# Performance work log

Hardware: AMD Instinct MI355X
Metric: run time of the kernel (lower is better)

Reference implementation:

```python
import jax, jax.numpy as jnp
import numpy as np

EPS_LN = 1e-5

def layer_norm(x, w, b):
    u = x.mean(-1, keepdims=True)
    s = jnp.mean((x - u) ** 2, -1, keepdims=True)
    return w * ((x - u) / jnp.sqrt(s + EPS_LN)) + b

def mlp(x, W, b, lw, lb):
    return jax.nn.relu(layer_norm(x @ W + b, lw, lb))

def mlp_gate(x, W, b, lw, lb):
    return jax.nn.sigmoid(layer_norm(x @ W + b, lw, lb))

def setup_inputs() -> dict:
    N, D = 768, 64
    key = jax.random.key(0)
    ks = jax.random.split(key, 12)
    inp = {
        'corr_index': jax.random.normal(ks[0], (N, N, 2), jnp.float32),
        'nei_index': jax.random.randint(ks[1], (N, N), 0, 2).astype(jnp.int64),
        'nei_num': jax.random.randint(ks[2], (N,), 0, N).astype(jnp.int64),
        'hidden_state': jax.random.normal(ks[3], (N, D), jnp.float32),
        'agent_v': jax.random.normal(ks[4], (N, 2), jnp.float32),
        # relativeLayer: MLP(3, D)
        'rel_w': jax.random.normal(ks[5], (3, D), jnp.float32) * (1.0 / np.sqrt(3)),
        'rel_b': jnp.zeros((D,), jnp.float32),
        'rel_lw': jnp.ones((D,), jnp.float32),
        'rel_lb': jnp.zeros((D,), jnp.float32),
        # ngate: MLP_gate(3D, D)
        'ng_w': jax.random.normal(ks[6], (3 * D, D), jnp.float32) * (1.0 / np.sqrt(3 * D)),
        'ng_b': jnp.zeros((D,), jnp.float32),
        'ng_lw': jnp.ones((D,), jnp.float32),
        'ng_lb': jnp.zeros((D,), jnp.float32),
        # WAr: MLP(3D, 1) -- LayerNorm(1) is identity in the source
        'war_w': jax.random.normal(ks[7], (3 * D, 1), jnp.float32) * (1.0 / np.sqrt(3 * D)),
        'war_b': jnp.zeros((1,), jnp.float32),
        # weight: MLP(D, D)
        'wt_w': jax.random.normal(ks[8], (D, D), jnp.float32) * (1.0 / np.sqrt(D)),
        'wt_b': jnp.zeros((D,), jnp.float32),
        'wt_lw': jnp.ones((D,), jnp.float32),
        'wt_lb': jnp.zeros((D,), jnp.float32),
    }
    return inp

def reference(corr_index, nei_index, nei_num, hidden_state, agent_v,
              rel_w, rel_b, rel_lw, rel_lb,
              ng_w, ng_b, ng_lw, ng_lb,
              war_w, war_b,
              wt_w, wt_b, wt_lw, wt_lb):
    N, D = hidden_state.shape
    # pair layout: row i*N+j  (i = receiver row of the NxN grid, j = column)
    agent_vt = jnp.tile(agent_v, (N, 1))                     # [N*N, 2], row i*N+j -> agent_v[j]
    corr_t = corr_index.reshape(N * N, 2)
    dot = agent_vt[:, 0] * corr_t[:, 0] + agent_vt[:, 1] * corr_t[:, 1]
    judge = jnp.sum(agent_vt ** 2, -1)
    angle = dot / (jnp.sqrt(judge * jnp.sum(corr_t ** 2, -1)) + 1e-10)
    angle = jnp.where(judge == 0, -1.0, angle)
    corr3 = jnp.concatenate([corr_t, angle[:, None]], -1)    # [N*N, 3]

    r_t = mlp(corr3, rel_w, rel_b, rel_lw, rel_lb)           # [N*N, D]
    nei_inputs = jnp.tile(hidden_state, (N, 1))              # row i*N+j -> h[j]
    hi_t = jnp.repeat(hidden_state, N, axis=0)               # row i*N+j -> h[i]
    tmp = jnp.concatenate([r_t, hi_t, nei_inputs], 1)        # [N*N, 3D]

    mask = (nei_index.reshape(N * N) > 0)
    nGate = mlp_gate(tmp, ng_w, ng_b, ng_lw, ng_lb)          # [N*N, D]
    tt = jax.nn.relu(tmp @ war_w + war_b).reshape(-1)        # LayerNorm(1) == identity

    Pos = jnp.where(mask, tt, 0.0).reshape(N, N)
    Pos = jnp.where(Pos == 0, -10000.0, Pos)
    Pos = jax.nn.softmax(Pos, axis=1)
    Pos_t = Pos.reshape(-1)

    H = jnp.where(mask[:, None], nei_inputs * nGate * Pos_t[:, None], 0.0)
    H_sum = mlp(H.reshape(N, N, D).sum(1), wt_w, wt_b, wt_lw, wt_lb)
    return hidden_state + H_sum
```

## Files before the change

### kernel.cpp

```cpp
#include <hip/hip_runtime.h>
#include <math.h>

#define NN 768
#define DD 64
#define WPB 8
#define TPW (NN / 16 / WPB)
#define RSTRIDE 34
#define PREBLKS 18

typedef _Float16 half8 __attribute__((ext_vector_type(8)));
typedef float    f32x4 __attribute__((ext_vector_type(4)));
typedef __fp16   p2f   __attribute__((ext_vector_type(2)));

union FragU { uint4 u4; unsigned int u[4]; half8 h; };
union PkU   { unsigned int u; p2f p; };

__device__ __forceinline__ unsigned int pk2(float a, float b) {
    PkU t; t.p = __builtin_amdgcn_cvt_pkrtz(a, b); return t.u;
}
__device__ __forceinline__ float lane_bcast(float v, int src) {
    return __int_as_float(__builtin_amdgcn_readlane(__float_as_int(v), src));
}
__device__ __forceinline__ f32x4 mfma16(FragU a, FragU b, f32x4 c) {
    return __builtin_amdgcn_mfma_f32_16x16x32_f16(a.h, b.h, c, 0, 0, 0);
}

__global__ __launch_bounds__(256) void k_prepack(
    const float* __restrict__ hs, const float* __restrict__ ng_w,
    const float* __restrict__ ng_b, const float* __restrict__ war_w,
    const float* __restrict__ war_b,
    const float* __restrict__ rel_w, const float* __restrict__ rel_b,
    const float* __restrict__ rel_lw, const float* __restrict__ rel_lb,
    float* __restrict__ sbase, float* __restrict__ warb, float* __restrict__ war3,
    unsigned int* __restrict__ hf16,
    unsigned int* __restrict__ afragS, unsigned int* __restrict__ afragR,
    float* __restrict__ mom)
{
    const int t = threadIdx.x, blk = blockIdx.x;
    const int lane = t & 63, q = t >> 6, g = lane >> 4, c16 = lane & 15;

    if (blk >= PREBLKS) {
        const int row = (blk - PREBLKS) * 4 + q;
        const float hv = hs[row * DD + lane];
        float a2 = ng_b[lane];
        #pragma unroll 8
        for (int k = 0; k < DD; ++k)
            a2 = fmaf(lane_bcast(hv, k), ng_w[(DD + k) * DD + lane], a2);
        sbase[row * DD + lane] = a2;
        float t2 = hv * war_w[DD + lane];
        float t3 = hv * war_w[2 * DD + lane];
        #pragma unroll
        for (int o = 32; o; o >>= 1) { t2 += __shfl_xor(t2, o); t3 += __shfl_xor(t3, o); }
        if (lane == 0) { warb[row] = t2 + war_b[0]; war3[row] = t3; }
        return;
    }

    for (int idx = blk * 256 + t; idx < NN * 32; idx += PREBLKS * 256) {
        const int row = idx >> 5, c = idx & 31;
        hf16[idx] = pk2(hs[row * DD + 2 * c], hs[row * DD + 2 * c + 1]);
    }

    if (blk < 16) {
        const int b = blk >> 2, c = blk & 3;
        const int dout = 16 * b + c16;
        const int k0 = 32 * c + g * 8 + 2 * q;
        const int r0 = (k0 < 64) ? k0 : (k0 + 64);
        afragS[(blk * 64 + lane) * 4 + q] =
            pk2(ng_w[r0 * DD + dout], ng_w[(r0 + 1) * DD + dout]);
    } else if (blk == 16) {
        const int b = q;
        const int d = 16 * b + c16;
        const float rlwd = rel_lw[d], rlbd = rel_lb[d];
        const float c0 = rel_w[d] * rlwd;
        const float c1 = rel_w[DD + d] * rlwd;
        const float c2 = rel_w[2 * DD + d] * rlwd;
        const float c3 = rel_b[d] * rlwd;
        PkU h01, h23, h45;
        h01.p = __builtin_amdgcn_cvt_pkrtz(c0, c1);
        h23.p = __builtin_amdgcn_cvt_pkrtz(c2, c3);
        h45.p = __builtin_amdgcn_cvt_pkrtz(rlwd, rlbd);
        const unsigned l01 = pk2(c0 - (float)h01.p[0], c1 - (float)h01.p[1]);
        const unsigned l23 = pk2(c2 - (float)h23.p[0], c3 - (float)h23.p[1]);
        const unsigned l45 = pk2(rlwd - (float)h45.p[0], rlbd - (float)h45.p[1]);
        const unsigned int base = (b * 64 + lane) * 4;
        unsigned v0, v1, v2;
        if (g == 0 || g == 1)      { v0 = h01.u; v1 = h23.u; v2 = h45.u; }
        else if (g == 2)           { v0 = l01;   v1 = l23;   v2 = l45;   }
        else                       { v0 = 0u;    v1 = 0u;    v2 = 0u;    }
        afragR[base + 0] = v0;
        afragR[base + 1] = v1;
        afragR[base + 2] = v2;
        afragR[base + 3] = 0u;
    } else {
        if (t < 64) {
            const float x0 = rel_w[t], x1 = rel_w[DD + t], x2 = rel_w[2 * DD + t];
            const float x3 = rel_b[t];
            float v[14] = {x0, x1, x2, x3,
                           x0 * x0, x1 * x1, x2 * x2, x3 * x3,
                           x0 * x1, x0 * x2, x0 * x3, x1 * x2, x1 * x3, x2 * x3};
            #pragma unroll
            for (int qq = 0; qq < 14; ++qq) {
                float s = v[qq];
                #pragma unroll
                for (int o = 32; o; o >>= 1) s += __shfl_xor(s, o);
                if (t == 0) mom[qq] = s * (1.f / 64.f);
            }
        }
    }
}

__global__ __launch_bounds__(512, 2) void k_main(
    const float* __restrict__ corr, const int* __restrict__ nei,
    const float* __restrict__ hs, const float* __restrict__ av,
    const float* __restrict__ ng_lw, const float* __restrict__ ng_lb,
    const float* __restrict__ war_w,
    const float* __restrict__ sbase, const float* __restrict__ warb,
    const float* __restrict__ war3,
    const unsigned int* __restrict__ afragS, const unsigned int* __restrict__ afragR,
    const unsigned int* __restrict__ hf16, const float* __restrict__ mom,
    float* __restrict__ Hsum)
{
    const int i = blockIdx.x;
    const int tid = threadIdx.x;
    const int lane = tid & 63, wave = tid >> 6;
    const int g = lane >> 4, c16 = lane & 15;

    __shared__ unsigned int smr[WPB * 16 * RSTRIDE];
    __shared__ float sm_red[WPB][DD];
    __shared__ float sm_m[WPB], sm_l[WPB];

    FragU aS[4][4], aR[4];
    #pragma unroll
    for (int b = 0; b < 4; ++b)
        #pragma unroll
        for (int c = 0; c < 4; ++c)
            aS[b][c].u4 = ((const uint4*)afragS)[(b * 4 + c) * 64 + lane];
    #pragma unroll
    for (int b = 0; b < 4; ++b) aR[b].u4 = ((const uint4*)afragR)[b * 64 + lane];

    float sb[16], nlwv[16], nlbv[16], wv16[16];
    #pragma unroll
    for (int b = 0; b < 4; ++b)
        #pragma unroll
        for (int r = 0; r < 4; ++r) {
            const int dout = 16 * b + g * 4 + r;
            sb[b * 4 + r]   = sbase[i * DD + dout];
            nlwv[b * 4 + r] = ng_lw[dout];
            nlbv[b * 4 + r] = ng_lb[dout];
            wv16[b * 4 + r] = war_w[dout];
        }

    const float m0 = mom[0], m1 = mom[1], m2 = mom[2], m3 = mom[3];
    const float M00 = mom[4], M11 = mom[5], M22 = mom[6], M33 = mom[7];
    const float M01 = mom[8], M02 = mom[9], M03 = mom[10];
    const float M12 = mom[11], M13 = mom[12], M23 = mom[13];

    const float warbase = warb[i];
    unsigned int* wrbase = smr + (wave * 16 + c16) * RSTRIDE;

    float acc[16];
    #pragma unroll
    for (int x = 0; x < 16; ++x) acc[x] = 0.f;
    float mrun = -INFINITY, lrun = 0.f;

    #pragma unroll 1
    for (int t = 0; t < TPW; ++t) {
        const int jj = 16 * (wave + WPB * t) + c16;
        const float2 cc = ((const float2*)corr)[i * NN + jj];
        const float2 vv = ((const float2*)av)[jj];
        const float cx = cc.x, cy = cc.y;
        const float judge = vv.x * vv.x + vv.y * vv.y;
        const float dotv = fmaf(vv.x, cx, vv.y * cy);
        const float cn = cx * cx + cy * cy;
        float angle = __fdividef(dotv, sqrtf(judge * cn) + 1e-10f);
        if (judge == 0.f) angle = -1.f;

        const float u = fmaf(cx, m0, fmaf(cy, m1, fmaf(angle, m2, m3)));
        float e2 = M33;
        e2 = fmaf(cx * cx, M00, e2);
        e2 = fmaf(cy * cy, M11, e2);
        e2 = fmaf(angle * angle, M22, e2);
        e2 = fmaf(2.f * cx, fmaf(cy, M01, fmaf(angle, M02, M03)), e2);
        e2 = fmaf(2.f * cy, fmaf(angle, M12, M13), e2);
        e2 = fmaf(2.f * angle, M23, e2);
        const float vare = (e2 - u * u) + 1e-5f;
        const float inv = rsqrtf(vare);
        const float sig = vare * inv;

        PkU s01, s23, s45;
        s01.p = __builtin_amdgcn_cvt_pkrtz(cx, cy);
        s23.p = __builtin_amdgcn_cvt_pkrtz(angle, 1.f);
        s45.p = __builtin_amdgcn_cvt_pkrtz(-u, sig);
        const unsigned l0 = pk2(cx - (float)s01.p[0], cy - (float)s01.p[1]);
        const unsigned l1 = pk2(angle - (float)s23.p[0], 0.f);
        const unsigned l2 = pk2((-u) - (float)s45.p[0], sig - (float)s45.p[1]);
        FragU b1;
        b1.u[0] = (g == 3) ? 0u : ((g == 1) ? l0 : s01.u);
        b1.u[1] = (g == 3) ? 0u : ((g == 1) ? l1 : s23.u);
        b1.u[2] = (g == 3) ? 0u : ((g == 1) ? l2 : s45.u);
        b1.u[3] = 0u;

        const f32x4 Z = {0.f, 0.f, 0.f, 0.f};
        float wd = 0.f;
        #pragma unroll
        for (int b = 0; b < 4; ++b) {
            const f32x4 P = mfma16(aR[b], b1, Z);
            const float r0f = fmaxf(P[0], 0.f) * inv;
            const float r1f = fmaxf(P[1], 0.f) * inv;
            const float r2f = fmaxf(P[2], 0.f) * inv;
            const float r3f = fmaxf(P[3], 0.f) * inv;
            wd = fmaf(r0f, wv16[b * 4 + 0], wd);
            wd = fmaf(r1f, wv16[b * 4 + 1], wd);
            wd = fmaf(r2f, wv16[b * 4 + 2], wd);
            wd = fmaf(r3f, wv16[b * 4 + 3], wd);
            uint2 wv;
            wv.x = pk2(r0f, r1f);
            wv.y = pk2(r2f, r3f);
            *(uint2*)(wrbase + 8 * b + 2 * g) = wv;
        }
        wd += __shfl_xor(wd, 16);
        wd += __shfl_xor(wd, 32);

        FragU bx0, bx1, bx2, bx3;
        {
            const uint2 lo0 = *(const uint2*)(wrbase + 4 * g);
            const uint2 hi0 = *(const uint2*)(wrbase + 4 * g + 2);
            bx0.u[0] = lo0.x; bx0.u[1] = lo0.y; bx0.u[2] = hi0.x; bx0.u[3] = hi0.y;
            const uint2 lo1 = *(const uint2*)(wrbase + 16 + 4 * g);
            const uint2 hi1 = *(const uint2*)(wrbase + 16 + 4 * g + 2);
            bx1.u[0] = lo1.x; bx1.u[1] = lo1.y; bx1.u[2] = hi1.x; bx1.u[3] = hi1.y;
        }
        bx2.u4 = *(const uint4*)(hf16 + jj * 32 + 4 * g);
        bx3.u4 = *(const uint4*)(hf16 + jj * 32 + 16 + 4 * g);

        f32x4 S[4];
        #pragma unroll
        for (int b = 0; b < 4; ++b) {
            f32x4 cinit = {sb[b * 4 + 0], sb[b * 4 + 1], sb[b * 4 + 2], sb[b * 4 + 3]};
            cinit = mfma16(aS[b][0], bx0, cinit);
            cinit = mfma16(aS[b][1], bx1, cinit);
            cinit = mfma16(aS[b][2], bx2, cinit);
            cinit = mfma16(aS[b][3], bx3, cinit);
            S[b] = cinit;
        }

        float s1 = 0.f, s2 = 0.f;
        #pragma unroll
        for (int x = 0; x < 16; ++x) {
            const float sv = S[x >> 2][x & 3];
            s1 += sv; s2 = fmaf(sv, sv, s2);
        }
        s1 += __shfl_xor(s1, 16); s1 += __shfl_xor(s1, 32);
        s2 += __shfl_xor(s2, 16); s2 += __shfl_xor(s2, 32);
        const float u2 = s1 * (1.f / 64.f);
        const float var2 = fmaf(s2, 1.f / 64.f, -u2 * u2);
        const float inv2 = rsqrtf(var2 + 1e-5f);

        float tt = wd + war3[jj] + warbase;
        tt = fmaxf(tt, 0.f);
        const bool msk = nei[i * NN + jj] > 0;
        const float p = (msk && tt > 0.f) ? tt : -10000.f;

        float pm = p;
        pm = fmaxf(pm, __shfl_xor(pm, 1));
        pm = fmaxf(pm, __shfl_xor(pm, 2));
        pm = fmaxf(pm, __shfl_xor(pm, 4));
        pm = fmaxf(pm, __shfl_xor(pm, 8));
        const float mn = fmaxf(mrun, pm);
        const float alpha = __expf(mrun - mn);
        const float e = __expf(p - mn);
        const float eacc = msk ? e : 0.f;
        lrun = fmaf(lrun, alpha, e);
        mrun = mn;

        #pragma unroll
        for (int b = 0; b < 4; ++b) {
            const f32x4 hv = *(const f32x4*)(hs + jj * DD + 16 * b + 4 * g);
            #pragma unroll
            for (int r = 0; r < 4; ++r) {
                const float ngv = fmaf((S[b][r] - u2) * inv2, nlwv[b * 4 + r],
                                       nlbv[b * 4 + r]);
                const float gate = __fdividef(1.f, 1.f + __expf(-ngv));
                acc[b * 4 + r] = fmaf(acc[b * 4 + r], alpha, eacc * gate * hv[r]);
            }
        }
    }

    #pragma unroll
    for (int o = 1; o <= 8; o <<= 1) {
        lrun += __shfl_xor(lrun, o);
        #pragma unroll
        for (int x = 0; x < 16; ++x) acc[x] += __shfl_xor(acc[x], o);
    }
    if (c16 == 0) {
        #pragma unroll
        for (int b = 0; b < 4; ++b)
            #pragma unroll
            for (int r = 0; r < 4; ++r)
                sm_red[wave][16 * b + g * 4 + r] = acc[b * 4 + r];
        if (lane == 0) { sm_m[wave] = mrun; sm_l[wave] = lrun; }
    }
    __syncthreads();
    if (tid < DD) {
        float M = sm_m[0];
        #pragma unroll
        for (int w = 1; w < WPB; ++w) M = fmaxf(M, sm_m[w]);
        float L = 0.f, A = 0.f;
        #pragma unroll
        for (int w = 0; w < WPB; ++w) {
            const float f = __expf(sm_m[w] - M);
            L = fmaf(sm_l[w], f, L);
            A = fmaf(sm_red[w][tid], f, A);
        }
        Hsum[i * DD + tid] = A / L;
    }
}

__global__ __launch_bounds__(256) void k_out(
    const float* __restrict__ Hsum, const float* __restrict__ hs,
    const float* __restrict__ wt_w, const float* __restrict__ wt_b,
    const float* __restrict__ wt_lw, const float* __restrict__ wt_lb,
    float* __restrict__ out)
{
    const int row = blockIdx.x * 4 + (threadIdx.x >> 6);
    const int lane = threadIdx.x & 63;
    const float hv = Hsum[row * DD + lane];
    float v = wt_b[lane];
    #pragma unroll 8
    for (int k = 0; k < DD; ++k)
        v = fmaf(lane_bcast(hv, k), wt_w[k * DD + lane], v);
    float s1 = v, s2 = v * v;
    #pragma unroll
    for (int o = 32; o; o >>= 1) { s1 += __shfl_xor(s1, o); s2 += __shfl_xor(s2, o); }
    const float u = s1 * (1.f / 64.f);
    const float var = fmaf(s2, 1.f / 64.f, -u * u);
    const float inv = rsqrtf(var + 1e-5f);
    const float r = fmaf((v - u) * inv, wt_lw[lane], wt_lb[lane]);
    out[row * DD + lane] = hs[row * DD + lane] + fmaxf(r, 0.f);
}

extern "C" void kernel_launch(void* const* d_in, const int* in_sizes, int n_in,
                              void* d_out, int out_size, void* d_ws, size_t ws_size,
                              hipStream_t stream) {
    const float* corr   = (const float*)d_in[0];
    const int*   nei    = (const int*)  d_in[1];
    const float* hs     = (const float*)d_in[3];
    const float* av     = (const float*)d_in[4];
    const float* rel_w  = (const float*)d_in[5];
    const float* rel_b  = (const float*)d_in[6];
    const float* rel_lw = (const float*)d_in[7];
    const float* rel_lb = (const float*)d_in[8];
    const float* ng_w   = (const float*)d_in[9];
    const float* ng_b   = (const float*)d_in[10];
    const float* ng_lw  = (const float*)d_in[11];
    const float* ng_lb  = (const float*)d_in[12];
    const float* war_w  = (const float*)d_in[13];
    const float* war_b  = (const float*)d_in[14];
    const float* wt_w   = (const float*)d_in[15];
    const float* wt_b   = (const float*)d_in[16];
    const float* wt_lw  = (const float*)d_in[17];
    const float* wt_lb  = (const float*)d_in[18];
    float* out = (float*)d_out;

    float* ws    = (float*)d_ws;
    float* sbase = ws;
    float* warb  = sbase + NN * DD;
    float* war3  = warb + NN;
    float* Hsum  = war3 + NN;
    float* mom   = Hsum + NN * DD;
    unsigned int* hf16   = (unsigned int*)(mom + 16);
    unsigned int* afragS = hf16 + NN * 32;
    unsigned int* afragR = afragS + 16 * 64 * 4;

    k_prepack<<<PREBLKS + NN / 4, 256, 0, stream>>>(
        hs, ng_w, ng_b, war_w, war_b, rel_w, rel_b, rel_lw, rel_lb,
        sbase, warb, war3, hf16, afragS, afragR, mom);
    k_main<<<NN, 64 * WPB, 0, stream>>>(
        corr, nei, hs, av, ng_lw, ng_lb, war_w, sbase, warb, war3,
        afragS, afragR, hf16, mom, Hsum);
    k_out<<<NN / 4, 256, 0, stream>>>(Hsum, hs, wt_w, wt_b, wt_lw, wt_lb, out);
}
```

Measured before the change: 166.5 us.

## Fuse output MLP into main kernel, prefetch next tile, halve waves per block

The final Hsum→MLP→residual kernel is folded into the tail of k_main, removing one launch and the Hsum round-trip through global memory. The main loop now software-prefetches the next tile's corr, agent_v, nei and war3 values and issues the hf16/hs loads at the top of the iteration to hide latency. Waves per block drop from 8 to 4, with launch bounds raised to 3 blocks per CU, so each wave processes twice as many tiles. The extra live registers from prefetching and the fused epilogue may raise register pressure, and the per-row epilogue runs on only one wave per block.

```diff
diff --git a/kernel.cpp b/kernel.cpp
--- a/kernel.cpp
+++ b/kernel.cpp
@@ -3,7 +3,7 @@
 
 #define NN 768
 #define DD 64
-#define WPB 8
+#define WPB 4
 #define TPW (NN / 16 / WPB)
 #define RSTRIDE 34
 #define PREBLKS 18
@@ -109,7 +109,7 @@
     }
 }
 
-__global__ __launch_bounds__(512, 2) void k_main(
+__global__ __launch_bounds__(64 * WPB, 3) void k_main(
     const float* __restrict__ corr, const int* __restrict__ nei,
     const float* __restrict__ hs, const float* __restrict__ av,
     const float* __restrict__ ng_lw, const float* __restrict__ ng_lb,
@@ -118,7 +118,9 @@
     const float* __restrict__ war3,
     const unsigned int* __restrict__ afragS, const unsigned int* __restrict__ afragR,
     const unsigned int* __restrict__ hf16, const float* __restrict__ mom,
-    float* __restrict__ Hsum)
+    const float* __restrict__ wt_w, const float* __restrict__ wt_b,
+    const float* __restrict__ wt_lw, const float* __restrict__ wt_lb,
+    float* __restrict__ out)
 {
     const int i = blockIdx.x;
     const int tid = threadIdx.x;
@@ -163,11 +165,29 @@
     for (int x = 0; x < 16; ++x) acc[x] = 0.f;
     float mrun = -INFINITY, lrun = 0.f;
 
+    int jj = 16 * wave + c16;
+    float2 cc = ((const float2*)corr)[i * NN + jj];
+    float2 vv = ((const float2*)av)[jj];
+    int    nv = nei[i * NN + jj];
+    float  w3 = war3[jj];
+
     #pragma unroll 1
     for (int t = 0; t < TPW; ++t) {
-        const int jj = 16 * (wave + WPB * t) + c16;
-        const float2 cc = ((const float2*)corr)[i * NN + jj];
-        const float2 vv = ((const float2*)av)[jj];
+        FragU bx2, bx3;
+        bx2.u4 = *(const uint4*)(hf16 + jj * 32 + 4 * g);
+        bx3.u4 = *(const uint4*)(hf16 + jj * 32 + 16 + 4 * g);
+        f32x4 hv0 = *(const f32x4*)(hs + jj * DD +  0 + 4 * g);
+        f32x4 hv1 = *(const f32x4*)(hs + jj * DD + 16 + 4 * g);
+        f32x4 hv2 = *(const f32x4*)(hs + jj * DD + 32 + 4 * g);
+        f32x4 hv3 = *(const f32x4*)(hs + jj * DD + 48 + 4 * g);
+
+        const int tn  = (t + 1 < TPW) ? (t + 1) : t;
+        const int jjn = 16 * (wave + WPB * tn) + c16;
+        const float2 cc_n = ((const float2*)corr)[i * NN + jjn];
+        const float2 vv_n = ((const float2*)av)[jjn];
+        const int    nv_n = nei[i * NN + jjn];
+        const float  w3_n = war3[jjn];
+
         const float cx = cc.x, cy = cc.y;
         const float judge = vv.x * vv.x + vv.y * vv.y;
         const float dotv = fmaf(vv.x, cx, vv.y * cy);
@@ -221,7 +241,7 @@
         wd += __shfl_xor(wd, 16);
         wd += __shfl_xor(wd, 32);
 
-        FragU bx0, bx1, bx2, bx3;
+        FragU bx0, bx1;
         {
             const uint2 lo0 = *(const uint2*)(wrbase + 4 * g);
             const uint2 hi0 = *(const uint2*)(wrbase + 4 * g + 2);
@@ -230,8 +250,6 @@
             const uint2 hi1 = *(const uint2*)(wrbase + 16 + 4 * g + 2);
             bx1.u[0] = lo1.x; bx1.u[1] = lo1.y; bx1.u[2] = hi1.x; bx1.u[3] = hi1.y;
         }
-        bx2.u4 = *(const uint4*)(hf16 + jj * 32 + 4 * g);
-        bx3.u4 = *(const uint4*)(hf16 + jj * 32 + 16 + 4 * g);
 
         f32x4 S[4];
         #pragma unroll
@@ -256,9 +274,9 @@
         const float var2 = fmaf(s2, 1.f / 64.f, -u2 * u2);
         const float inv2 = rsqrtf(var2 + 1e-5f);
 
-        float tt = wd + war3[jj] + warbase;
+        float tt = wd + w3 + warbase;
         tt = fmaxf(tt, 0.f);
-        const bool msk = nei[i * NN + jj] > 0;
+        const bool msk = nv > 0;
         const float p = (msk && tt > 0.f) ? tt : -10000.f;
 
         float pm = p;
@@ -275,15 +293,17 @@
 
         #pragma unroll
         for (int b = 0; b < 4; ++b) {
-            const f32x4 hv = *(const f32x4*)(hs + jj * DD + 16 * b + 4 * g);
+            const f32x4 hvb = (b == 0) ? hv0 : (b == 1) ? hv1 : (b == 2) ? hv2 : hv3;
             #pragma unroll
             for (int r = 0; r < 4; ++r) {
                 const float ngv = fmaf((S[b][r] - u2) * inv2, nlwv[b * 4 + r],
                                        nlbv[b * 4 + r]);
                 const float gate = __fdividef(1.f, 1.f + __expf(-ngv));
-                acc[b * 4 + r] = fmaf(acc[b * 4 + r], alpha, eacc * gate * hv[r]);
+                acc[b * 4 + r] = fmaf(acc[b * 4 + r], alpha, eacc * gate * hvb[r]);
             }
         }
+
+        jj = jjn; cc = cc_n; vv = vv_n; nv = nv_n; w3 = w3_n;
     }
 
     #pragma unroll
@@ -301,6 +321,7 @@
         if (lane == 0) { sm_m[wave] = mrun; sm_l[wave] = lrun; }
     }
     __syncthreads();
+
     if (tid < DD) {
         float M = sm_m[0];
         #pragma unroll
@@ -312,31 +333,20 @@
             L = fmaf(sm_l[w], f, L);
             A = fmaf(sm_red[w][tid], f, A);
         }
-        Hsum[i * DD + tid] = A / L;
-    }
-}
-
-__global__ __launch_bounds__(256) void k_out(
-    const float* __restrict__ Hsum, const float* __restrict__ hs,
-    const float* __restrict__ wt_w, const float* __restrict__ wt_b,
-    const float* __restrict__ wt_lw, const float* __restrict__ wt_lb,
-    float* __restrict__ out)
-{
-    const int row = blockIdx.x * 4 + (threadIdx.x >> 6);
-    const int lane = threadIdx.x & 63;
-    const float hv = Hsum[row * DD + lane];
-    float v = wt_b[lane];
-    #pragma unroll 8
-    for (int k = 0; k < DD; ++k)
-        v = fmaf(lane_bcast(hv, k), wt_w[k * DD + lane], v);
-    float s1 = v, s2 = v * v;
-    #pragma unroll
-    for (int o = 32; o; o >>= 1) { s1 += __shfl_xor(s1, o); s2 += __shfl_xor(s2, o); }
-    const float u = s1 * (1.f / 64.f);
-    const float var = fmaf(s2, 1.f / 64.f, -u * u);
-    const float inv = rsqrtf(var + 1e-5f);
-    const float r = fmaf((v - u) * inv, wt_lw[lane], wt_lb[lane]);
-    out[row * DD + lane] = hs[row * DD + lane] + fmaxf(r, 0.f);
+        const float Hv = A / L;
+        float v = wt_b[tid];
+        #pragma unroll 8
+        for (int k = 0; k < DD; ++k)
+            v = fmaf(lane_bcast(Hv, k), wt_w[k * DD + tid], v);
+        float t1 = v, t2 = v * v;
+        #pragma unroll
+        for (int o = 32; o; o >>= 1) { t1 += __shfl_xor(t1, o); t2 += __shfl_xor(t2, o); }
+        const float uo = t1 * (1.f / 64.f);
+        const float varo = fmaf(t2, 1.f / 64.f, -uo * uo);
+        const float invo = rsqrtf(varo + 1e-5f);
+        const float ro = fmaf((v - uo) * invo, wt_lw[tid], wt_lb[tid]);
+        out[i * DD + tid] = hs[i * DD + tid] + fmaxf(ro, 0.f);
+    }
 }
 
 extern "C" void kernel_launch(void* const* d_in, const int* in_sizes, int n_in,
@@ -366,8 +376,7 @@
     float* sbase = ws;
     float* warb  = sbase + NN * DD;
     float* war3  = warb + NN;
-    float* Hsum  = war3 + NN;
-    float* mom   = Hsum + NN * DD;
+    float* mom   = war3 + NN;
     unsigned int* hf16   = (unsigned int*)(mom + 16);
     unsigned int* afragS = hf16 + NN * 32;
     unsigned int* afragR = afragS + 16 * 64 * 4;
@@ -377,6 +386,5 @@
         sbase, warb, war3, hf16, afragS, afragR, mom);
     k_main<<<NN, 64 * WPB, 0, stream>>>(
         corr, nei, hs, av, ng_lw, ng_lb, war_w, sbase, warb, war3,
-        afragS, afragR, hf16, mom, Hsum);
-    k_out<<<NN / 4, 256, 0, stream>>>(Hsum, hs, wt_w, wt_b, wt_lw, wt_lb, out);
-}
+        afragS, afragR, hf16, mom, wt_w, wt_b, wt_lw, wt_lb, out);
+}
```

After: 205.8 us. 1.24x slower.
